# Kernel optimization log

Measured on AMD Instinct MI355X. Metric: run time of the kernel, lower is better.

The kernel has to match this reference:

```python
import jax, jax.numpy as jnp
import numpy as np

MIN_LEN = 4
MAX_LEN = 32
N = 55440 * 1024  # 56,770,560 elements, ~227 MB fp32; divisible by many lengths in [4,32]


def _candidate_lengths(n, min_len, max_len):
    # Static (Python-level) replication of the torch loop's candidate set:
    # pattern_len in range(min_len, min(max_len+1, n//2)) with n % pattern_len == 0
    return [L for L in range(min_len, min(max_len + 1, n // 2)) if n % L == 0]

CAND_LENS = _candidate_lengths(N, MIN_LEN, MAX_LEN)  # 20 candidate lengths


def setup_inputs() -> dict:
    key = jax.random.key(0)
    x = jax.random.normal(key, (N,), dtype=jnp.float32)
    return {"x": x}


def reference(x):
    """Faithful jax version of PyTorchPatternMatcher.find_patterns.

    Instead of a dict with data-dependent contents, returns fixed-shape arrays:
      max_diffs[k]  : max |reshaped - first_pattern| for candidate length CAND_LENS[k]
      eff_scores[k] : (n // L) / L if max_diff < 0.01 else 0 (torch's score, gated)
      best_idx      : argmax of eff_scores (index of the best pattern, if any)
      best_score    : eff_scores[best_idx] (0.0 means no pattern found)
    """
    flat = x.reshape(-1)
    n = flat.shape[0]  # static
    max_diffs = []
    raw_scores = []
    for L in CAND_LENS:  # small static set (~20), not a data-dim loop
        r = flat.reshape(-1, L)                 # [n//L, L]
        md = jnp.max(jnp.abs(r - r[0]))         # segment-max-diff vs first pattern
        max_diffs.append(md)
        raw_scores.append(float(n // L) / float(L))
    max_diffs = jnp.stack(max_diffs)                               # [K]
    raw_scores = jnp.asarray(raw_scores, dtype=jnp.float32)        # [K]
    valid = max_diffs < 0.01
    eff_scores = jnp.where(valid, raw_scores, jnp.float32(0.0))    # [K]
    best_idx = jnp.argmax(eff_scores)
    best_score = eff_scores[best_idx]
    return max_diffs, eff_scores, best_idx, best_score
```

## Files before the change

### kernel.cpp

```cpp
#include <hip/hip_runtime.h>
#include <hip/hip_bf16.h>

#define N_TOTAL 56770560
#define PCOLS   110880
#define NROWS   512
#define C4      27720
#define NLENS   20
#define SPL     16
#define SPAN    (PCOLS / SPL)
#define RC      16

typedef float floatx4 __attribute__((ext_vector_type(4)));

__constant__ int kLens[NLENS] = {4,5,6,7,8,9,10,11,12,14,15,16,18,20,21,22,24,28,30,32};

__global__ __launch_bounds__(256) void colminmax_kernel(
    const floatx4* __restrict__ x, float* __restrict__ pmax,
    float* __restrict__ pmin) {
  const int rowsPerChunk = NROWS / RC;
  int c4 = blockIdx.x * 256 + threadIdx.x;
  if (c4 >= C4) return;
  int chunk = blockIdx.y;
  const floatx4* p = x + (size_t)chunk * rowsPerChunk * C4 + c4;

  floatx4 vmx = {-3.402823466e38f, -3.402823466e38f,
                 -3.402823466e38f, -3.402823466e38f};
  floatx4 vmn = {3.402823466e38f, 3.402823466e38f,
                 3.402823466e38f, 3.402823466e38f};
#pragma unroll 8
  for (int r = 0; r < rowsPerChunk; ++r) {
    floatx4 v = __builtin_nontemporal_load(&p[(size_t)r * C4]);
    vmx.x = fmaxf(vmx.x, v.x); vmn.x = fminf(vmn.x, v.x);
    vmx.y = fmaxf(vmx.y, v.y); vmn.y = fminf(vmn.y, v.y);
    vmx.z = fmaxf(vmx.z, v.z); vmn.z = fminf(vmn.z, v.z);
    vmx.w = fmaxf(vmx.w, v.w); vmn.w = fminf(vmn.w, v.w);
  }
  ((floatx4*)(pmax + (size_t)chunk * PCOLS))[c4] = vmx;
  ((floatx4*)(pmin + (size_t)chunk * PCOLS))[c4] = vmn;
}

__global__ __launch_bounds__(256) void fold_kernel(
    const float* __restrict__ pmax, const float* __restrict__ pmin,
    float* __restrict__ Mx, float* __restrict__ Mn) {
  int r = blockIdx.x * 256 + threadIdx.x;
  if (r >= PCOLS) return;
  float mx = pmax[r], mn = pmin[r];
#pragma unroll
  for (int c = 1; c < RC; ++c) {
    mx = fmaxf(mx, pmax[(size_t)c * PCOLS + r]);
    mn = fminf(mn, pmin[(size_t)c * PCOLS + r]);
  }
  Mx[r] = mx;
  Mn[r] = mn;
}

__global__ __launch_bounds__(256) void md_kernel(
    const float* __restrict__ x, const float* __restrict__ Mx,
    const float* __restrict__ Mn, float* __restrict__ mdpart) {
  __shared__ float pat[32];
  __shared__ float red[4];
  const int tid = threadIdx.x;
  const int L = kLens[blockIdx.y];
  const int base = blockIdx.x * SPAN;
  if (tid < 32) pat[tid] = x[tid];
  __syncthreads();

  int s = 256 % L;
  int rm = (base + tid) % L;
  float acc = 0.0f;
#pragma unroll 5
  for (int r = base + tid; r < base + SPAN; r += 256) {
    float p = pat[rm];
    acc = fmaxf(acc, fmaxf(Mx[r] - p, p - Mn[r]));
    rm += s;
    if (rm >= L) rm -= L;
  }
#pragma unroll
  for (int off = 32; off > 0; off >>= 1)
    acc = fmaxf(acc, __shfl_down(acc, off, 64));
  if ((tid & 63) == 0) red[tid >> 6] = acc;
  __syncthreads();
  if (tid == 0) {
    mdpart[blockIdx.y * SPL + blockIdx.x] =
        fmaxf(fmaxf(red[0], red[1]), fmaxf(red[2], red[3]));
  }
}

__global__ void fin_kernel(const float* __restrict__ mdpart,
                           float* __restrict__ out) {
  __shared__ float eff_s[NLENS];
  const int k = threadIdx.x;
  if (k < NLENS) {
    float md = 0.0f;
#pragma unroll
    for (int j = 0; j < SPL; ++j) md = fmaxf(md, mdpart[k * SPL + j]);
    out[k] = md;
    const int L = kLens[k];
    double raw = (double)(N_TOTAL / L) / (double)L;
    float eff = (md < 0.01f) ? (float)raw : 0.0f;
    out[NLENS + k] = eff;
    eff_s[k] = eff;
  }
  __syncthreads();
  if (k == 0) {
    float best = eff_s[0];
    int bi = 0;
    for (int i = 1; i < NLENS; ++i) {
      if (eff_s[i] > best) { best = eff_s[i]; bi = i; }
    }
    out[2 * NLENS] = (float)bi;
    out[2 * NLENS + 1] = best;
  }
}

extern "C" void kernel_launch(void* const* d_in, const int* in_sizes, int n_in,
                              void* d_out, int out_size, void* d_ws, size_t ws_size,
                              hipStream_t stream) {
  const float* x = (const float*)d_in[0];
  float* out = (float*)d_out;

  float* Mx     = (float*)d_ws;
  float* Mn     = Mx + PCOLS;
  float* pmax   = Mn + PCOLS;
  float* pmin   = pmax + (size_t)RC * PCOLS;
  float* mdpart = pmin + (size_t)RC * PCOLS;

  dim3 grid1((C4 + 255) / 256, RC);
  colminmax_kernel<<<grid1, 256, 0, stream>>>((const floatx4*)x, pmax, pmin);
  fold_kernel<<<(PCOLS + 255) / 256, 256, 0, stream>>>(pmax, pmin, Mx, Mn);
  dim3 grid3(SPL, NLENS);
  md_kernel<<<grid3, 256, 0, stream>>>(x, Mx, Mn, mdpart);
  fin_kernel<<<1, 64, 0, stream>>>(mdpart, out);
}
```

Baseline: 298.2 us.

## Process two column vectors per thread and fuse finalize into md kernel

Each thread in the column min/max pass now handles two floatx4 columns, which halves the grid and doubles the loads in flight per thread. The finalize kernel is folded into md_kernel: a last-block-done atomic counter, reset inside fold_kernel, picks the block that computes the scores and argmax. Fold loads become nontemporal. This removes one kernel launch and aims to raise memory-level parallelism, at the cost of fewer resident waves and an atomic/threadfence handshake.

Result: no change. 303.5 us (+1.8%).

```diff
diff --git a/kernel.cpp b/kernel.cpp
--- a/kernel.cpp
+++ b/kernel.cpp
@@ -5,10 +5,12 @@
 #define PCOLS   110880
 #define NROWS   512
 #define C4      27720
+#define C4H     13860
 #define NLENS   20
 #define SPL     16
 #define SPAN    (PCOLS / SPL)
 #define RC      16
+#define NMDBLK  (SPL * NLENS)
 
 typedef float floatx4 __attribute__((ext_vector_type(4)));
 
@@ -19,36 +21,49 @@
     float* __restrict__ pmin) {
   const int rowsPerChunk = NROWS / RC;
   int c4 = blockIdx.x * 256 + threadIdx.x;
-  if (c4 >= C4) return;
+  if (c4 >= C4H) return;
   int chunk = blockIdx.y;
-  const floatx4* p = x + (size_t)chunk * rowsPerChunk * C4 + c4;
+  const floatx4* p0 = x + (size_t)chunk * rowsPerChunk * C4 + c4;
+  const floatx4* p1 = p0 + C4H;
 
-  floatx4 vmx = {-3.402823466e38f, -3.402823466e38f,
+  floatx4 mx0 = {-3.402823466e38f, -3.402823466e38f,
                  -3.402823466e38f, -3.402823466e38f};
-  floatx4 vmn = {3.402823466e38f, 3.402823466e38f,
+  floatx4 mx1 = mx0;
+  floatx4 mn0 = {3.402823466e38f, 3.402823466e38f,
                  3.402823466e38f, 3.402823466e38f};
+  floatx4 mn1 = mn0;
 #pragma unroll 8
   for (int r = 0; r < rowsPerChunk; ++r) {
-    floatx4 v = __builtin_nontemporal_load(&p[(size_t)r * C4]);
-    vmx.x = fmaxf(vmx.x, v.x); vmn.x = fminf(vmn.x, v.x);
-    vmx.y = fmaxf(vmx.y, v.y); vmn.y = fminf(vmn.y, v.y);
-    vmx.z = fmaxf(vmx.z, v.z); vmn.z = fminf(vmn.z, v.z);
-    vmx.w = fmaxf(vmx.w, v.w); vmn.w = fminf(vmn.w, v.w);
+    floatx4 v0 = __builtin_nontemporal_load(&p0[(size_t)r * C4]);
+    floatx4 v1 = __builtin_nontemporal_load(&p1[(size_t)r * C4]);
+    mx0.x = fmaxf(mx0.x, v0.x); mn0.x = fminf(mn0.x, v0.x);
+    mx0.y = fmaxf(mx0.y, v0.y); mn0.y = fminf(mn0.y, v0.y);
+    mx0.z = fmaxf(mx0.z, v0.z); mn0.z = fminf(mn0.z, v0.z);
+    mx0.w = fmaxf(mx0.w, v0.w); mn0.w = fminf(mn0.w, v0.w);
+    mx1.x = fmaxf(mx1.x, v1.x); mn1.x = fminf(mn1.x, v1.x);
+    mx1.y = fmaxf(mx1.y, v1.y); mn1.y = fminf(mn1.y, v1.y);
+    mx1.z = fmaxf(mx1.z, v1.z); mn1.z = fminf(mn1.z, v1.z);
+    mx1.w = fmaxf(mx1.w, v1.w); mn1.w = fminf(mn1.w, v1.w);
   }
-  ((floatx4*)(pmax + (size_t)chunk * PCOLS))[c4] = vmx;
-  ((floatx4*)(pmin + (size_t)chunk * PCOLS))[c4] = vmn;
+  floatx4* omx = (floatx4*)(pmax + (size_t)chunk * PCOLS);
+  floatx4* omn = (floatx4*)(pmin + (size_t)chunk * PCOLS);
+  omx[c4] = mx0; omx[c4 + C4H] = mx1;
+  omn[c4] = mn0; omn[c4 + C4H] = mn1;
 }
 
 __global__ __launch_bounds__(256) void fold_kernel(
     const float* __restrict__ pmax, const float* __restrict__ pmin,
-    float* __restrict__ Mx, float* __restrict__ Mn) {
+    float* __restrict__ Mx, float* __restrict__ Mn,
+    unsigned int* __restrict__ cnt) {
+  if (blockIdx.x == 0 && threadIdx.x == 0) *cnt = 0u;
   int r = blockIdx.x * 256 + threadIdx.x;
   if (r >= PCOLS) return;
-  float mx = pmax[r], mn = pmin[r];
+  float mx = __builtin_nontemporal_load(&pmax[r]);
+  float mn = __builtin_nontemporal_load(&pmin[r]);
 #pragma unroll
   for (int c = 1; c < RC; ++c) {
-    mx = fmaxf(mx, pmax[(size_t)c * PCOLS + r]);
-    mn = fminf(mn, pmin[(size_t)c * PCOLS + r]);
+    mx = fmaxf(mx, __builtin_nontemporal_load(&pmax[(size_t)c * PCOLS + r]));
+    mn = fminf(mn, __builtin_nontemporal_load(&pmin[(size_t)c * PCOLS + r]));
   }
   Mx[r] = mx;
   Mn[r] = mn;
@@ -56,9 +71,12 @@
 
 __global__ __launch_bounds__(256) void md_kernel(
     const float* __restrict__ x, const float* __restrict__ Mx,
-    const float* __restrict__ Mn, float* __restrict__ mdpart) {
+    const float* __restrict__ Mn, float* __restrict__ mdpart,
+    unsigned int* __restrict__ cnt, float* __restrict__ out) {
   __shared__ float pat[32];
   __shared__ float red[4];
+  __shared__ int isLast_s;
+  __shared__ float eff_s[NLENS];
   const int tid = threadIdx.x;
   const int L = kLens[blockIdx.y];
   const int base = blockIdx.x * SPAN;
@@ -83,26 +101,28 @@
   if (tid == 0) {
     mdpart[blockIdx.y * SPL + blockIdx.x] =
         fmaxf(fmaxf(red[0], red[1]), fmaxf(red[2], red[3]));
+    __threadfence();
+    unsigned int t = atomicAdd(cnt, 1u);
+    isLast_s = (t == NMDBLK - 1u) ? 1 : 0;
   }
-}
+  __syncthreads();
+  if (!isLast_s) return;
 
-__global__ void fin_kernel(const float* __restrict__ mdpart,
-                           float* __restrict__ out) {
-  __shared__ float eff_s[NLENS];
-  const int k = threadIdx.x;
+  __threadfence();
+  const int k = tid;
   if (k < NLENS) {
     float md = 0.0f;
 #pragma unroll
     for (int j = 0; j < SPL; ++j) md = fmaxf(md, mdpart[k * SPL + j]);
     out[k] = md;
-    const int L = kLens[k];
-    double raw = (double)(N_TOTAL / L) / (double)L;
+    const int Lk = kLens[k];
+    double raw = (double)(N_TOTAL / Lk) / (double)Lk;
     float eff = (md < 0.01f) ? (float)raw : 0.0f;
     out[NLENS + k] = eff;
     eff_s[k] = eff;
   }
   __syncthreads();
-  if (k == 0) {
+  if (tid == 0) {
     float best = eff_s[0];
     int bi = 0;
     for (int i = 1; i < NLENS; ++i) {
@@ -124,11 +144,11 @@
   float* pmax   = Mn + PCOLS;
   float* pmin   = pmax + (size_t)RC * PCOLS;
   float* mdpart = pmin + (size_t)RC * PCOLS;
+  unsigned int* cnt = (unsigned int*)(mdpart + NMDBLK);
 
-  dim3 grid1((C4 + 255) / 256, RC);
+  dim3 grid1((C4H + 255) / 256, RC);
   colminmax_kernel<<<grid1, 256, 0, stream>>>((const floatx4*)x, pmax, pmin);
-  fold_kernel<<<(PCOLS + 255) / 256, 256, 0, stream>>>(pmax, pmin, Mx, Mn);
+  fold_kernel<<<(PCOLS + 255) / 256, 256, 0, stream>>>(pmax, pmin, Mx, Mn, cnt);
   dim3 grid3(SPL, NLENS);
-  md_kernel<<<grid3, 256, 0, stream>>>(x, Mx, Mn, mdpart);
-  fin_kernel<<<1, 64, 0, stream>>>(mdpart, out);
+  md_kernel<<<grid3, 256, 0, stream>>>(x, Mx, Mn, mdpart, cnt, out);
 }
```
